# Optimization experiments

Measured on AMD Instinct MI355X. Metric: run time of the kernel, lower is better.

## Reference

```python
import jax, jax.numpy as jnp
import numpy as np

L, H, HS, D, T, V, B = 6, 6, 64, 384, 256, 65, 64
EPS = 1e-5


def layer_norm(x, g, b):
    m = x.mean(-1, keepdims=True)
    v = x.var(-1, keepdims=True)
    return (x - m) / jnp.sqrt(v + EPS) * g + b


def setup_inputs() -> dict:
    key = jax.random.key(0)
    ks = jax.random.split(key, 12)
    s = 0.02
    return {
        "idx": jax.random.randint(ks[0], (B, T), 0, V),
        "targets": jax.random.randint(ks[1], (B, T), 0, V),
        "tok_emb": s * jax.random.normal(ks[2], (V, D), jnp.float32),
        "pos_emb": s * jax.random.normal(ks[3], (T, D), jnp.float32),
        "Wq": s * jax.random.normal(ks[4], (L, H, D, HS), jnp.float32),
        "Wk": s * jax.random.normal(ks[5], (L, H, D, HS), jnp.float32),
        "Wv": s * jax.random.normal(ks[6], (L, H, D, HS), jnp.float32),
        "Wproj": s * jax.random.normal(ks[7], (L, D, D), jnp.float32),
        "bproj": jnp.zeros((L, D), jnp.float32),
        "W1": s * jax.random.normal(ks[8], (L, D, 4 * D), jnp.float32),
        "b1": jnp.zeros((L, 4 * D), jnp.float32),
        "W2": s * jax.random.normal(ks[9], (L, 4 * D, D), jnp.float32),
        "b2": jnp.zeros((L, D), jnp.float32),
        "ln1_g": jnp.ones((L, D), jnp.float32),
        "ln1_b": jnp.zeros((L, D), jnp.float32),
        "lnf_g": jnp.ones((D,), jnp.float32),
        "lnf_b": jnp.zeros((D,), jnp.float32),
        "Whead": s * jax.random.normal(ks[10], (D, V), jnp.float32),
        "bhead": jnp.zeros((V,), jnp.float32),
    }


def reference(idx, targets, tok_emb, pos_emb, Wq, Wk, Wv, Wproj, bproj,
              W1, b1, W2, b2, ln1_g, ln1_b, lnf_g, lnf_b, Whead, bhead):
    b, t = idx.shape
    x = tok_emb[idx] + pos_emb[:t]  # [B,T,D]
    mask = jnp.tril(jnp.ones((t, t), bool))
    scale = x.shape[-1] ** -0.5  # NOTE: original scales by n_emb_d**-0.5, not head_size**-0.5
    for l in range(L):
        y = layer_norm(x, ln1_g[l], ln1_b[l])
        q = jnp.einsum('btd,hde->bhte', y, Wq[l])
        k = jnp.einsum('btd,hde->bhte', y, Wk[l])
        v = jnp.einsum('btd,hde->bhte', y, Wv[l])
        w = jnp.einsum('bhte,bhse->bhts', q, k) * scale
        w = jnp.where(mask, w, -jnp.inf)
        w = jax.nn.softmax(w, axis=-1)
        o = jnp.einsum('bhts,bhse->bhte', w, v)
        o = o.transpose(0, 2, 1, 3).reshape(b, t, H * HS)  # concat heads on last dim
        x = x + o @ Wproj[l] + bproj[l]
        # NOTE: original Block reuses ln1 (not ln2) before the FFN -- replicated faithfully
        y2 = layer_norm(x, ln1_g[l], ln1_b[l])
        x = x + jax.nn.relu(y2 @ W1[l] + b1[l]) @ W2[l] + b2[l]
    x = layer_norm(x, lnf_g, lnf_b)
    logits = x @ Whead + bhead  # [B,T,V]
    logp = jax.nn.log_softmax(logits, axis=-1)
    loss = -jnp.take_along_axis(logp, targets[..., None], axis=-1).mean()
    return logits, loss
```

## Files before the change

### kernel.cpp

```cpp
#include <hip/hip_runtime.h>
#include <math.h>

#define L_ 6
#define H_ 6
#define HS_ 64
#define D_ 384
#define T_ 256
#define V_ 65
#define B_ 64
#define ROWS (B_*T_)
#define QKVN 1152
#define EPS_ 1e-5f

typedef __attribute__((ext_vector_type(8))) __bf16 bf16x8;
typedef __attribute__((ext_vector_type(2))) __bf16 bf16x2;
typedef __attribute__((ext_vector_type(4))) float f32x4;

__device__ __forceinline__ bf16x8 u4_to_bf8(uint4 u) {
    return __builtin_bit_cast(bf16x8, u);
}

__device__ __forceinline__ void glds16(const void* g, void* l) {
    __builtin_amdgcn_global_load_lds(
        (const __attribute__((address_space(1))) void*)g,
        (__attribute__((address_space(3))) void*)l, 16, 0, 0);
}

__global__ __launch_bounds__(256)
void embed_kernel(const int* __restrict__ idx,
                  const float* __restrict__ tok,
                  const float* __restrict__ pos,
                  float* __restrict__ x) {
    int i = blockIdx.x * blockDim.x + threadIdx.x;
    int e = i * 4;
    int d = e % D_;
    int row = e / D_;
    int t = row % T_;
    const float4 tv = *(const float4*)(tok + (size_t)idx[row]*D_ + d);
    const float4 pv = *(const float4*)(pos + (size_t)t*D_ + d);
    float4 r;
    r.x = tv.x + pv.x; r.y = tv.y + pv.y;
    r.z = tv.z + pv.z; r.w = tv.w + pv.w;
    *(float4*)(x + e) = r;
}

__global__ __launch_bounds__(256)
void ln4(const float* __restrict__ x,
         const float* __restrict__ g,
         const float* __restrict__ b,
         __bf16* __restrict__ yb) {
    int w = threadIdx.x >> 6, lane = threadIdx.x & 63;
    int row = blockIdx.x * 4 + w;
    const float* xr = x + (size_t)row * D_;
    float2 v[3];
    #pragma unroll
    for (int i = 0; i < 3; ++i) v[i] = *(const float2*)(xr + lane*2 + 128*i);
    float s = 0.f, sq = 0.f;
    #pragma unroll
    for (int i = 0; i < 3; ++i) {
        s += v[i].x + v[i].y;
        sq += v[i].x*v[i].x + v[i].y*v[i].y;
    }
    for (int off = 32; off; off >>= 1) {
        s  += __shfl_xor(s,  off);
        sq += __shfl_xor(sq, off);
    }
    float mean = s * (1.0f/D_);
    float var  = sq * (1.0f/D_) - mean*mean;
    float rstd = rsqrtf(var + EPS_);
    __bf16* yr = yb + (size_t)row * D_;
    #pragma unroll
    for (int i = 0; i < 3; ++i) {
        int c = lane*2 + 128*i;
        float2 gv = *(const float2*)(g + c);
        float2 bv = *(const float2*)(b + c);
        bf16x2 pr;
        pr[0] = (__bf16)((v[i].x-mean)*rstd*gv.x + bv.x);
        pr[1] = (__bf16)((v[i].y-mean)*rstd*gv.y + bv.y);
        *(bf16x2*)(yr + c) = pr;
    }
}

__global__ __launch_bounds__(256)
void transpose_cast(const float* __restrict__ src, __bf16* __restrict__ dst,
                    int R, int C, int zdiv, long sA, long sB, long dbase)
{
    __shared__ float tile[32][33];
    int z = blockIdx.z;
    const float* s = src + (long)z * R * C;
    __bf16* d = dst + dbase + (long)(z / zdiv) * sA + (long)(z % zdiv) * sB;
    int c0 = blockIdx.x * 32, r0 = blockIdx.y * 32;
    int t = threadIdx.x;
    int tr = t >> 3, tc = (t & 7) * 4;
    float4 v = *(const float4*)(s + (long)(r0 + tr) * C + c0 + tc);
    tile[tr][tc+0] = v.x; tile[tr][tc+1] = v.y;
    tile[tr][tc+2] = v.z; tile[tr][tc+3] = v.w;
    __syncthreads();
    #pragma unroll
    for (int j = 0; j < 4; ++j)
        d[(long)(c0 + tr) * R + r0 + tc + j] = (__bf16)tile[tc+j][tr];
}

__global__ __launch_bounds__(256)
void head_prep(const float* __restrict__ Whead, __bf16* __restrict__ headT) {
    int i = blockIdx.x * 256 + threadIdx.x;
    int n = i / D_, k = i % D_;
    headT[i] = (n < V_) ? (__bf16)Whead[k*V_ + n] : (__bf16)0.0f;
}

template<int TM>
__global__ __launch_bounds__(256)
void gemm_t(const __bf16* __restrict__ A, const __bf16* __restrict__ Bt,
            const float* __restrict__ bias, const float* res,
            float* outF, __bf16* outB,
            int K, int ldc, int ncols, int relu)
{
    constexpr int MI = TM / 32;
    __shared__ __align__(16) __bf16 As[2][TM*32];
    __shared__ __align__(16) __bf16 Bs[2][128*32];
    int t = threadIdx.x;
    int w = t >> 6, lane = t & 63;
    int ln = lane & 15, quad = lane >> 4;
    int n0 = blockIdx.x * 128, m0 = blockIdx.y * TM;
    int wm = (w >> 1) * (TM/2), wn = (w & 1) * 64;

    f32x4 acc[MI][4] = {};

    const char* Ab = (const char*)A + (size_t)m0 * K * 2;
    const char* Bb = (const char*)Bt + (size_t)n0 * K * 2;
    int f0 = w*64 + lane, f1 = f0 + 256;
    int r0 = f0 >> 2, r1 = f1 >> 2;
    size_t ga0 = (size_t)r0 * K * 2 + (size_t)(((f0 & 3) ^ (r0 & 3)) * 16);
    size_t ga1 = (size_t)r1 * K * 2 + (size_t)(((f1 & 3) ^ (r1 & 3)) * 16);
    int lo0 = w*64*16, lo1 = (w*64 + 256)*16;

    int nIt = K >> 5;
    glds16(Ab + ga0, (char*)As[0] + lo0);
    if constexpr (TM == 128) glds16(Ab + ga1, (char*)As[0] + lo1);
    glds16(Bb + ga0, (char*)Bs[0] + lo0);
    glds16(Bb + ga1, (char*)Bs[0] + lo1);

    for (int it = 0; it < nIt; ++it) {
        int p = it & 1;
        __syncthreads();
        if (it + 1 < nIt) {
            size_t kb = (size_t)(it + 1) * 64;
            glds16(Ab + ga0 + kb, (char*)As[p^1] + lo0);
            if constexpr (TM == 128) glds16(Ab + ga1 + kb, (char*)As[p^1] + lo1);
            glds16(Bb + ga0 + kb, (char*)Bs[p^1] + lo0);
            glds16(Bb + ga1 + kb, (char*)Bs[p^1] + lo1);
        }
        bf16x8 af[MI], bfr[4];
        #pragma unroll
        for (int i = 0; i < MI; ++i) {
            int row = wm + i*16 + ln;
            af[i] = __builtin_bit_cast(bf16x8,
                *(const uint4*)&As[p][row*32 + ((quad ^ (row & 3)) * 8)]);
        }
        #pragma unroll
        for (int j = 0; j < 4; ++j) {
            int row = wn + j*16 + ln;
            bfr[j] = __builtin_bit_cast(bf16x8,
                *(const uint4*)&Bs[p][row*32 + ((quad ^ (row & 3)) * 8)]);
        }
        #pragma unroll
        for (int i = 0; i < MI; ++i)
            #pragma unroll
            for (int j = 0; j < 4; ++j)
                acc[i][j] = __builtin_amdgcn_mfma_f32_16x16x32_bf16(
                                af[i], bfr[j], acc[i][j], 0, 0, 0);
    }
    #pragma unroll
    for (int i = 0; i < MI; ++i) {
        #pragma unroll
        for (int r = 0; r < 4; ++r) {
            int row = m0 + wm + i*16 + quad*4 + r;
            #pragma unroll
            for (int j = 0; j < 4; ++j) {
                int col = n0 + wn + j*16 + ln;
                if (col < ncols) {
                    float v = acc[i][j][r];
                    if (bias) v += bias[col];
                    if (relu) v = fmaxf(v, 0.f);
                    if (res)  v += res[(size_t)row*ldc + col];
                    if (outF) outF[(size_t)row*ldc + col] = v;
                    if (outB) outB[(size_t)row*ldc + col] = (__bf16)v;
                }
            }
        }
    }
}

__global__ __launch_bounds__(256, 2)
void attn4(const __bf16* __restrict__ qkv, __bf16* __restrict__ o)
{
    __shared__ __align__(16) __bf16 Ks[256*72];
    __shared__ __align__(16) __bf16 Vt[64*264];
    __shared__ __align__(16) __bf16 Pw[4][32*40];
    int bid = blockIdx.x;
    int h = bid % H_;
    int b = bid / H_;
    int t = threadIdx.x;
    int w = t >> 6, lane = t & 63;
    int ln = lane & 15, quad = lane >> 4;
    const size_t rowb = (size_t)b * T_ * QKVN;
    const int hoff = h * HS_;
    const float scale = 0.05103103630798288f;

    for (int c = t; c < 2048; c += 256) {
        int r = c >> 3, e0 = (c & 7) * 8;
        uint4 uk = *(const uint4*)(qkv + rowb + (size_t)r*QKVN + 384 + hoff + e0);
        *(uint4*)&Ks[r*72 + e0] = uk;
        uint4 uv = *(const uint4*)(qkv + rowb + (size_t)r*QKVN + 768 + hoff + e0);
        bf16x8 v8 = u4_to_bf8(uv);
        #pragma unroll
        for (int j = 0; j < 8; ++j) {
            int e = e0 + j;
            Vt[e*264 + (((r >> 3) ^ ((e >> 3) & 3)) * 8) + (r & 7)] = v8[j];
        }
    }

    int qis[2] = { w, 7 - w };
    uint4 Qf[2][2][2];
    #pragma unroll
    for (int tl = 0; tl < 2; ++tl)
        #pragma unroll
        for (int mi = 0; mi < 2; ++mi)
            #pragma unroll
            for (int kc = 0; kc < 2; ++kc)
                Qf[tl][mi][kc] = *(const uint4*)(qkv + rowb +
                    (size_t)(qis[tl]*32 + mi*16 + ln)*QKVN + hoff + kc*32 + quad*8);

    __syncthreads();

    __bf16* P = Pw[w];
    #pragma unroll
    for (int tl = 0; tl < 2; ++tl) {
        int qi = qis[tl];
        f32x4 O[2][4] = {};
        float mst[2][4], lst[2][4];
        #pragma unroll
        for (int mi = 0; mi < 2; ++mi)
            #pragma unroll
            for (int r = 0; r < 4; ++r) { mst[mi][r] = -INFINITY; lst[mi][r] = 0.f; }

        for (int st = 0; st <= qi; ++st) {
            int sb = st * 32;
            f32x4 S[2][2] = {};
            #pragma unroll
            for (int kc = 0; kc < 2; ++kc) {
                uint4 Kf[2];
                #pragma unroll
                for (int ji = 0; ji < 2; ++ji)
                    Kf[ji] = *(const uint4*)&Ks[(sb + ji*16 + ln)*72 + kc*32 + quad*8];
                __builtin_amdgcn_s_setprio(1);
                #pragma unroll
                for (int mi = 0; mi < 2; ++mi) {
                    bf16x8 qa = __builtin_bit_cast(bf16x8, Qf[tl][mi][kc]);
                    #pragma unroll
                    for (int ji = 0; ji < 2; ++ji)
                        S[mi][ji] = __builtin_amdgcn_mfma_f32_16x16x32_bf16(
                            qa, __builtin_bit_cast(bf16x8, Kf[ji]), S[mi][ji], 0, 0, 0);
                }
                __builtin_amdgcn_s_setprio(0);
            }
            int diag = (st == qi);
            #pragma unroll
            for (int mi = 0; mi < 2; ++mi)
                #pragma unroll
                for (int ji = 0; ji < 2; ++ji)
                    #pragma unroll
                    for (int r = 0; r < 4; ++r) {
                        float v = S[mi][ji][r] * scale;
                        if (diag && (ji*16 + ln) > (mi*16 + quad*4 + r)) v = -INFINITY;
                        S[mi][ji][r] = v;
                    }
            #pragma unroll
            for (int mi = 0; mi < 2; ++mi)
                #pragma unroll
                for (int r = 0; r < 4; ++r) {
                    float mx = fmaxf(S[mi][0][r], S[mi][1][r]);
                    #pragma unroll
                    for (int off = 1; off < 16; off <<= 1)
                        mx = fmaxf(mx, __shfl_xor(mx, off));
                    float mn = fmaxf(mst[mi][r], mx);
                    float al = __expf(mst[mi][r] - mn);
                    mst[mi][r] = mn;
                    float p0 = __expf(S[mi][0][r] - mn);
                    float p1 = __expf(S[mi][1][r] - mn);
                    S[mi][0][r] = p0; S[mi][1][r] = p1;
                    float rs = p0 + p1;
                    #pragma unroll
                    for (int off = 1; off < 16; off <<= 1)
                        rs += __shfl_xor(rs, off);
                    lst[mi][r] = lst[mi][r]*al + rs;
                    #pragma unroll
                    for (int ei = 0; ei < 4; ++ei) O[mi][ei][r] *= al;
                }
            #pragma unroll
            for (int mi = 0; mi < 2; ++mi)
                #pragma unroll
                for (int ji = 0; ji < 2; ++ji)
                    #pragma unroll
                    for (int r = 0; r < 4; ++r)
                        P[(mi*16 + quad*4 + r)*40 + ji*16 + ln] = (__bf16)S[mi][ji][r];
            uint4 Pf[2], Vf[4];
            #pragma unroll
            for (int mi = 0; mi < 2; ++mi)
                Pf[mi] = *(const uint4*)&P[(mi*16 + ln)*40 + quad*8];
            #pragma unroll
            for (int ei = 0; ei < 4; ++ei) {
                int e = ei*16 + ln;
                Vf[ei] = *(const uint4*)&Vt[e*264 + (((st*4 + quad) ^ ((e >> 3) & 3)) * 8)];
            }
            __builtin_amdgcn_s_setprio(1);
            #pragma unroll
            for (int mi = 0; mi < 2; ++mi)
                #pragma unroll
                for (int ei = 0; ei < 4; ++ei)
                    O[mi][ei] = __builtin_amdgcn_mfma_f32_16x16x32_bf16(
                        __builtin_bit_cast(bf16x8, Pf[mi]),
                        __builtin_bit_cast(bf16x8, Vf[ei]), O[mi][ei], 0, 0, 0);
            __builtin_amdgcn_s_setprio(0);
        }
        #pragma unroll
        for (int mi = 0; mi < 2; ++mi)
            #pragma unroll
            for (int r = 0; r < 4; ++r) {
                float inv = 1.0f / lst[mi][r];
                size_t row = (size_t)(b*T_ + qi*32 + mi*16 + quad*4 + r);
                #pragma unroll
                for (int ei = 0; ei < 4; ++ei)
                    o[row*D_ + hoff + ei*16 + ln] = (__bf16)(O[mi][ei][r] * inv);
            }
    }
}

__global__ __launch_bounds__(256)
void loss2(const float* __restrict__ logits,
           const int* __restrict__ tg,
           float* __restrict__ loss)
{
    int t = threadIdx.x;
    int g16 = t >> 4, ln = t & 15;
    int row = blockIdx.x * 16 + g16;
    const float* lr = logits + (size_t)row * V_;
    float v0 = lr[ln], v1 = lr[16+ln], v2 = lr[32+ln], v3 = lr[48+ln];
    float v4 = (ln == 0) ? lr[64] : -INFINITY;
    float m = fmaxf(fmaxf(fmaxf(v0, v1), fmaxf(v2, v3)), v4);
    #pragma unroll
    for (int off = 1; off < 16; off <<= 1) m = fmaxf(m, __shfl_xor(m, off));
    float s = __expf(v0-m) + __expf(v1-m) + __expf(v2-m) + __expf(v3-m);
    if (ln == 0) s += __expf(v4-m);
    #pragma unroll
    for (int off = 1; off < 16; off <<= 1) s += __shfl_xor(s, off);
    float val = 0.f;
    if (ln == 0)
        val = -(lr[tg[row]] - m - __logf(s)) * (1.0f/ROWS);
    #pragma unroll
    for (int off = 16; off < 64; off <<= 1) val += __shfl_xor(val, off);
    __shared__ float red[4];
    int w = t >> 6;
    if ((t & 63) == 0) red[w] = val;
    __syncthreads();
    if (t == 0)
        atomicAdd(loss, red[0]+red[1]+red[2]+red[3]);
}

extern "C" void kernel_launch(void* const* d_in, const int* in_sizes, int n_in,
                              void* d_out, int out_size, void* d_ws, size_t ws_size,
                              hipStream_t stream)
{
    const int*   idx     = (const int*)  d_in[0];
    const int*   targets = (const int*)  d_in[1];
    const float* tok     = (const float*)d_in[2];
    const float* pos     = (const float*)d_in[3];
    const float* Wq      = (const float*)d_in[4];
    const float* Wk      = (const float*)d_in[5];
    const float* Wv      = (const float*)d_in[6];
    const float* Wproj   = (const float*)d_in[7];
    const float* bproj   = (const float*)d_in[8];
    const float* W1      = (const float*)d_in[9];
    const float* b1      = (const float*)d_in[10];
    const float* W2      = (const float*)d_in[11];
    const float* b2      = (const float*)d_in[12];
    const float* ln1g    = (const float*)d_in[13];
    const float* ln1b    = (const float*)d_in[14];
    const float* lnfg    = (const float*)d_in[15];
    const float* lnfb    = (const float*)d_in[16];
    const float* Whead   = (const float*)d_in[17];
    const float* bhead   = (const float*)d_in[18];

    float* logits = (float*)d_out;
    float* loss   = logits + (size_t)ROWS * V_;

    const size_t SZ = (size_t)ROWS * D_;
    const size_t RGELEMS = (size_t)ROWS * 4 * D_;

    float*  x   = (float*)d_ws;
    __bf16* yb  = (__bf16*)(x + SZ);
    __bf16* Rg  = yb + SZ;
    __bf16* qkv = Rg;
    __bf16* hid = Rg;
    __bf16* o   = Rg + RGELEMS;
    __bf16* qkvT  = o + SZ;
    __bf16* projT = qkvT + (size_t)L_*QKVN*D_;
    __bf16* w1T   = projT + (size_t)L_*D_*D_;
    __bf16* w2T   = w1T + (size_t)L_*D_*4*D_;
    __bf16* headT = w2T + (size_t)L_*D_*4*D_;

    transpose_cast<<<dim3(2,12,36),256,0,stream>>>(Wq, qkvT, D_, HS_, H_,
        (long)QKVN*D_, (long)HS_*D_, 0L);
    transpose_cast<<<dim3(2,12,36),256,0,stream>>>(Wk, qkvT, D_, HS_, H_,
        (long)QKVN*D_, (long)HS_*D_, (long)D_*D_);
    transpose_cast<<<dim3(2,12,36),256,0,stream>>>(Wv, qkvT, D_, HS_, H_,
        (long)QKVN*D_, (long)HS_*D_, 2L*D_*D_);
    transpose_cast<<<dim3(12,12,6),256,0,stream>>>(Wproj, projT, D_, D_, 1,
        (long)D_*D_, 0L, 0L);
    transpose_cast<<<dim3(48,12,6),256,0,stream>>>(W1, w1T, D_, 4*D_, 1,
        (long)D_*4*D_, 0L, 0L);
    transpose_cast<<<dim3(12,48,6),256,0,stream>>>(W2, w2T, 4*D_, D_, 1,
        (long)D_*4*D_, 0L, 0L);
    head_prep<<<(128*D_)/256, 256, 0, stream>>>(Whead, headT);

    embed_kernel<<<(ROWS*D_/4)/256, 256, 0, stream>>>(idx, tok, pos, x);

    for (int l = 0; l < L_; ++l) {
        ln4<<<ROWS/4, 256, 0, stream>>>(x, ln1g + l*D_, ln1b + l*D_, yb);
        gemm_t<128><<<dim3(QKVN/128, ROWS/128), 256, 0, stream>>>(
            yb, qkvT + (size_t)l*QKVN*D_, nullptr, nullptr, nullptr, qkv,
            D_, QKVN, QKVN, 0);
        attn4<<<B_*H_, 256, 0, stream>>>(qkv, o);
        gemm_t<64><<<dim3(D_/128, ROWS/64), 256, 0, stream>>>(
            o, projT + (size_t)l*D_*D_, bproj + l*D_, x, x, nullptr,
            D_, D_, D_, 0);
        ln4<<<ROWS/4, 256, 0, stream>>>(x, ln1g + l*D_, ln1b + l*D_, yb);
        gemm_t<128><<<dim3(4*D_/128, ROWS/128), 256, 0, stream>>>(
            yb, w1T + (size_t)l*D_*4*D_, b1 + l*4*D_, nullptr, nullptr, hid,
            D_, 4*D_, 4*D_, 1);
        gemm_t<64><<<dim3(D_/128, ROWS/64), 256, 0, stream>>>(
            hid, w2T + (size_t)l*D_*4*D_, b2 + l*D_, x, x, nullptr,
            4*D_, D_, D_, 0);
    }
    ln4<<<ROWS/4, 256, 0, stream>>>(x, lnfg, lnfb, yb);
    gemm_t<64><<<dim3(1, ROWS/64), 256, 0, stream>>>(
        yb, headT, bhead, nullptr, logits, nullptr,
        D_, V_, V_, 0);
    hipMemsetAsync(loss, 0, sizeof(float), stream);
    loss2<<<ROWS/16, 256, 0, stream>>>(logits, targets, loss);
}
```

Before: 1.530 ms.

## Add triple-buffered BK=64 GEMM for narrow-N residual matmuls with M-major grid

Splits the templated GEMM into a 128x128 kernel and a new 64x128 kernel for the proj, FFN2 and head matmuls. The new kernel uses a K-tile of 64 with three LDS buffers, explicit vmcnt waits and raw barriers so two tiles are in flight, plus an 8-way XOR swizzle. Its grid is reordered so blockIdx.x walks M, letting neighbouring blocks share the same weight tile in cache. The trade-off is more LDS per block (about 72 KB), which may lower occupancy, and hand-tuned wait counts that depend on the exact number of loads issued.

```diff
diff --git a/kernel.cpp b/kernel.cpp
--- a/kernel.cpp
+++ b/kernel.cpp
@@ -108,23 +108,21 @@
     headT[i] = (n < V_) ? (__bf16)Whead[k*V_ + n] : (__bf16)0.0f;
 }
 
-template<int TM>
-__global__ __launch_bounds__(256)
-void gemm_t(const __bf16* __restrict__ A, const __bf16* __restrict__ Bt,
-            const float* __restrict__ bias, const float* res,
-            float* outF, __bf16* outB,
-            int K, int ldc, int ncols, int relu)
+__global__ __launch_bounds__(256)
+void gemm128(const __bf16* __restrict__ A, const __bf16* __restrict__ Bt,
+             const float* __restrict__ bias,
+             float* outF, __bf16* outB,
+             int K, int ldc, int ncols, int relu)
 {
-    constexpr int MI = TM / 32;
-    __shared__ __align__(16) __bf16 As[2][TM*32];
+    __shared__ __align__(16) __bf16 As[2][128*32];
     __shared__ __align__(16) __bf16 Bs[2][128*32];
     int t = threadIdx.x;
     int w = t >> 6, lane = t & 63;
     int ln = lane & 15, quad = lane >> 4;
-    int n0 = blockIdx.x * 128, m0 = blockIdx.y * TM;
-    int wm = (w >> 1) * (TM/2), wn = (w & 1) * 64;
-
-    f32x4 acc[MI][4] = {};
+    int n0 = blockIdx.x * 128, m0 = blockIdx.y * 128;
+    int wm = (w >> 1) * 64, wn = (w & 1) * 64;
+
+    f32x4 acc[4][4] = {};
 
     const char* Ab = (const char*)A + (size_t)m0 * K * 2;
     const char* Bb = (const char*)Bt + (size_t)n0 * K * 2;
@@ -136,7 +134,7 @@
 
     int nIt = K >> 5;
     glds16(Ab + ga0, (char*)As[0] + lo0);
-    if constexpr (TM == 128) glds16(Ab + ga1, (char*)As[0] + lo1);
+    glds16(Ab + ga1, (char*)As[0] + lo1);
     glds16(Bb + ga0, (char*)Bs[0] + lo0);
     glds16(Bb + ga1, (char*)Bs[0] + lo1);
 
@@ -146,13 +144,13 @@
         if (it + 1 < nIt) {
             size_t kb = (size_t)(it + 1) * 64;
             glds16(Ab + ga0 + kb, (char*)As[p^1] + lo0);
-            if constexpr (TM == 128) glds16(Ab + ga1 + kb, (char*)As[p^1] + lo1);
+            glds16(Ab + ga1 + kb, (char*)As[p^1] + lo1);
             glds16(Bb + ga0 + kb, (char*)Bs[p^1] + lo0);
             glds16(Bb + ga1 + kb, (char*)Bs[p^1] + lo1);
         }
-        bf16x8 af[MI], bfr[4];
-        #pragma unroll
-        for (int i = 0; i < MI; ++i) {
+        bf16x8 af[4], bfr[4];
+        #pragma unroll
+        for (int i = 0; i < 4; ++i) {
             int row = wm + i*16 + ln;
             af[i] = __builtin_bit_cast(bf16x8,
                 *(const uint4*)&As[p][row*32 + ((quad ^ (row & 3)) * 8)]);
@@ -164,14 +162,123 @@
                 *(const uint4*)&Bs[p][row*32 + ((quad ^ (row & 3)) * 8)]);
         }
         #pragma unroll
-        for (int i = 0; i < MI; ++i)
+        for (int i = 0; i < 4; ++i)
             #pragma unroll
             for (int j = 0; j < 4; ++j)
                 acc[i][j] = __builtin_amdgcn_mfma_f32_16x16x32_bf16(
                                 af[i], bfr[j], acc[i][j], 0, 0, 0);
     }
     #pragma unroll
-    for (int i = 0; i < MI; ++i) {
+    for (int i = 0; i < 4; ++i) {
+        #pragma unroll
+        for (int r = 0; r < 4; ++r) {
+            int row = m0 + wm + i*16 + quad*4 + r;
+            #pragma unroll
+            for (int j = 0; j < 4; ++j) {
+                int col = n0 + wn + j*16 + ln;
+                if (col < ncols) {
+                    float v = acc[i][j][r];
+                    if (bias) v += bias[col];
+                    if (relu) v = fmaxf(v, 0.f);
+                    if (outF) outF[(size_t)row*ldc + col] = v;
+                    if (outB) outB[(size_t)row*ldc + col] = (__bf16)v;
+                }
+            }
+        }
+    }
+}
+
+__global__ __launch_bounds__(256)
+void gemm64(const __bf16* __restrict__ A, const __bf16* __restrict__ Bt,
+            const float* __restrict__ bias, const float* res,
+            float* outF, __bf16* outB,
+            int K, int ldc, int ncols, int relu)
+{
+    __shared__ __align__(16) __bf16 As[3][64*64];
+    __shared__ __align__(16) __bf16 Bs[3][128*64];
+    int t = threadIdx.x;
+    int w = t >> 6, lane = t & 63;
+    int ln = lane & 15, quad = lane >> 4;
+    int m0 = blockIdx.x * 64, n0 = blockIdx.y * 128;
+    int wm = (w >> 1) * 32, wn = (w & 1) * 64;
+
+    f32x4 acc[2][4] = {};
+
+    const char* Ab = (const char*)A + (size_t)m0 * K * 2;
+    const char* Bb = (const char*)Bt + (size_t)n0 * K * 2;
+    int fb = w*64 + lane;
+    size_t gaA[2]; int loA[2];
+    #pragma unroll
+    for (int ra = 0; ra < 2; ++ra) {
+        int f = fb + 256*ra;
+        gaA[ra] = (size_t)(f >> 3) * (K*2) + (size_t)(((f & 7) ^ ((f >> 3) & 7)) * 16);
+        loA[ra] = f * 16;
+    }
+    size_t gaB[4]; int loB[4];
+    #pragma unroll
+    for (int rb = 0; rb < 4; ++rb) {
+        int f = fb + 256*rb;
+        gaB[rb] = (size_t)(f >> 3) * (K*2) + (size_t)(((f & 7) ^ ((f >> 3) & 7)) * 16);
+        loB[rb] = f * 16;
+    }
+
+    int nIt = K >> 6;
+
+    #define STAGE64(buf, itv) do {                                         \
+        size_t kb_ = (size_t)(itv) * 128;                                  \
+        _Pragma("unroll")                                                  \
+        for (int ra = 0; ra < 2; ++ra)                                     \
+            glds16(Ab + gaA[ra] + kb_, (char*)As[buf] + loA[ra]);          \
+        _Pragma("unroll")                                                  \
+        for (int rb = 0; rb < 4; ++rb)                                     \
+            glds16(Bb + gaB[rb] + kb_, (char*)Bs[buf] + loB[rb]);          \
+    } while (0)
+
+    STAGE64(0, 0);
+    STAGE64(1, 1);
+
+    for (int it = 0; it < nIt; ++it) {
+        int p = it % 3;
+        if (it + 1 < nIt)
+            asm volatile("s_waitcnt vmcnt(6)" ::: "memory");
+        else
+            asm volatile("s_waitcnt vmcnt(0)" ::: "memory");
+        __builtin_amdgcn_s_barrier();
+        __builtin_amdgcn_sched_barrier(0);
+        if (it + 2 < nIt) {
+            int q = p + 2; if (q >= 3) q -= 3;
+            STAGE64(q, it + 2);
+        }
+        bf16x8 af[2][2], bfr[4][2];
+        #pragma unroll
+        for (int i = 0; i < 2; ++i) {
+            int row = wm + i*16 + ln;
+            #pragma unroll
+            for (int kk = 0; kk < 2; ++kk)
+                af[i][kk] = __builtin_bit_cast(bf16x8,
+                    *(const uint4*)&As[p][row*64 + (((kk*4 + quad) ^ (row & 7)) * 8)]);
+        }
+        #pragma unroll
+        for (int j = 0; j < 4; ++j) {
+            int row = wn + j*16 + ln;
+            #pragma unroll
+            for (int kk = 0; kk < 2; ++kk)
+                bfr[j][kk] = __builtin_bit_cast(bf16x8,
+                    *(const uint4*)&Bs[p][row*64 + (((kk*4 + quad) ^ (row & 7)) * 8)]);
+        }
+        #pragma unroll
+        for (int kk = 0; kk < 2; ++kk)
+            #pragma unroll
+            for (int i = 0; i < 2; ++i)
+                #pragma unroll
+                for (int j = 0; j < 4; ++j)
+                    acc[i][j] = __builtin_amdgcn_mfma_f32_16x16x32_bf16(
+                                    af[i][kk], bfr[j][kk], acc[i][j], 0, 0, 0);
+    }
+    #undef STAGE64
+
+    #pragma unroll
+    for (int i = 0; i < 2; ++i) {
         #pragma unroll
         for (int r = 0; r < 4; ++r) {
             int row = m0 + wm + i*16 + quad*4 + r;
@@ -427,23 +534,23 @@
 
     for (int l = 0; l < L_; ++l) {
         ln4<<<ROWS/4, 256, 0, stream>>>(x, ln1g + l*D_, ln1b + l*D_, yb);
-        gemm_t<128><<<dim3(QKVN/128, ROWS/128), 256, 0, stream>>>(
-            yb, qkvT + (size_t)l*QKVN*D_, nullptr, nullptr, nullptr, qkv,
+        gemm128<<<dim3(QKVN/128, ROWS/128), 256, 0, stream>>>(
+            yb, qkvT + (size_t)l*QKVN*D_, nullptr, nullptr, qkv,
             D_, QKVN, QKVN, 0);
         attn4<<<B_*H_, 256, 0, stream>>>(qkv, o);
-        gemm_t<64><<<dim3(D_/128, ROWS/64), 256, 0, stream>>>(
+        gemm64<<<dim3(ROWS/64, D_/128), 256, 0, stream>>>(
             o, projT + (size_t)l*D_*D_, bproj + l*D_, x, x, nullptr,
             D_, D_, D_, 0);
         ln4<<<ROWS/4, 256, 0, stream>>>(x, ln1g + l*D_, ln1b + l*D_, yb);
-        gemm_t<128><<<dim3(4*D_/128, ROWS/128), 256, 0, stream>>>(
-            yb, w1T + (size_t)l*D_*4*D_, b1 + l*4*D_, nullptr, nullptr, hid,
+        gemm128<<<dim3(4*D_/128, ROWS/128), 256, 0, stream>>>(
+            yb, w1T + (size_t)l*D_*4*D_, b1 + l*4*D_, nullptr, hid,
             D_, 4*D_, 4*D_, 1);
-        gemm_t<64><<<dim3(D_/128, ROWS/64), 256, 0, stream>>>(
+        gemm64<<<dim3(ROWS/64, D_/128), 256, 0, stream>>>(
             hid, w2T + (size_t)l*D_*4*D_, b2 + l*D_, x, x, nullptr,
             4*D_, D_, D_, 0);
     }
     ln4<<<ROWS/4, 256, 0, stream>>>(x, lnfg, lnfb, yb);
-    gemm_t<64><<<dim3(1, ROWS/64), 256, 0, stream>>>(
+    gemm64<<<dim3(ROWS/64, 1), 256, 0, stream>>>(
         yb, headT, bhead, nullptr, logits, nullptr,
         D_, V_, V_, 0);
     hipMemsetAsync(loss, 0, sizeof(float), stream);
```

New measurement: 1.727 ms. 1.13x slower.
